# Kernel tuning notes

Measured on AMD Instinct MI355X. Metric: run time of the kernel, lower is better.

Reference implementation:

```python
import jax, jax.numpy as jnp
import numpy as np


def setup_inputs() -> dict:
    key = jax.random.key(0)
    k1, k2 = jax.random.split(key)
    B, D, H, W = 16, 64, 64, 64
    K = 1024  # codebook_size
    x = jax.random.normal(k1, (B, D, H, W), dtype=jnp.float32)
    codebook = jax.random.normal(k2, (K, D), dtype=jnp.float32)
    return {"x": x, "codebook": codebook}


def reference(x, codebook):
    """VQ quantization: nearest-codebook lookup.

    x: (B, D, H, W) latent features; codebook: (K, D).
    Returns (quantized (B, D, H, W), indices (B, H, W)).
    """
    B, D, H, W = x.shape
    # (B, D, H, W) -> (B*H*W, D)
    flat = jnp.transpose(x, (0, 2, 3, 1)).reshape(-1, D)
    d2 = (
        jnp.sum(flat * flat, axis=-1, keepdims=True)
        - 2.0 * (flat @ codebook.T)
        + jnp.sum(codebook * codebook, axis=-1)
    )
    idx = jnp.argmin(d2, axis=-1)  # (N,)
    quantized = codebook[idx]  # (N, D) gather
    quantized = quantized.reshape(B, H, W, D).transpose(0, 3, 1, 2)
    return quantized, idx.reshape(B, H, W)
```

## Files before the change

kernel.cpp:

```cpp
#include <hip/hip_runtime.h>
#include <hip/hip_bf16.h>

#define D_ 64
#define HW_ 4096
#define K_ 1024
#define NPTS_ 65536
#define QOUT_ 4194304
#define DELTA 0.006f
#define INF_ 3.4e38f
#define KSPL 4
#define KPB  256

typedef short bf16x8 __attribute__((ext_vector_type(8)));
typedef float f32x4 __attribute__((ext_vector_type(4)));

__device__ __forceinline__ void gload_lds16(const float* g, float* l) {
    __builtin_amdgcn_global_load_lds((const __attribute__((address_space(1))) void*)g,
                                     (__attribute__((address_space(3))) void*)l, 16, 0, 0);
}
__device__ __forceinline__ void gload_lds4(const float* g, float* l) {
    __builtin_amdgcn_global_load_lds((const __attribute__((address_space(1))) void*)g,
                                     (__attribute__((address_space(3))) void*)l, 4, 0, 0);
}

__global__ __launch_bounds__(256) void vq_pack(const float* __restrict__ cb,
                                               float* __restrict__ cnorm,
                                               short* __restrict__ P) {
    const int t = blockIdx.x * 256 + threadIdx.x;
    const int gch = t >> 6, l = t & 63;
    const int j  = gch * 16 + (l & 15);
    const int dg = l >> 4;
#pragma unroll
    for (int s = 0; s < 2; ++s) {
        const float* src = cb + j * D_ + s * 32 + dg * 8;
        short hb[8], lb[8];
#pragma unroll
        for (int i = 0; i < 8; ++i) {
            const float v = -2.f * src[i];
            __hip_bfloat16 h = __float2bfloat16(v);
            hb[i] = *(const short*)&h;
            const float r = v - __bfloat162float(h);
            __hip_bfloat16 lo = __float2bfloat16(r);
            lb[i] = *(const short*)&lo;
        }
        short* dh = P + ((size_t)((gch * 2 + s) * 2 + 0) * 64 + l) * 8;
        short* dl = P + ((size_t)((gch * 2 + s) * 2 + 1) * 64 + l) * 8;
#pragma unroll
        for (int i = 0; i < 8; ++i) { dh[i] = hb[i]; dl[i] = lb[i]; }
    }
    if (t < K_) {
        const float4* r = (const float4*)(cb + (size_t)t * D_);
        float s0 = 0.f, s1 = 0.f, s2 = 0.f, s3 = 0.f;
#pragma unroll
        for (int i = 0; i < 16; ++i) {
            float4 v = r[i];
            s0 = fmaf(v.x, v.x, s0); s1 = fmaf(v.y, v.y, s1);
            s2 = fmaf(v.z, v.z, s2); s3 = fmaf(v.w, v.w, s3);
        }
        cnorm[t] = (s0 + s1) + (s2 + s3);
    }
}

__global__ __launch_bounds__(512, 4) void vq_main(const float* __restrict__ x,
                                                  const float* __restrict__ cnorm_g,
                                                  const short* __restrict__ P,
                                                  float* __restrict__ out) {
    __shared__ short cbuf[16 * 2 * 2 * 64 * 8];
    __shared__ float cnt[KPB];

    const int tid  = threadIdx.x;
    const int lane = tid & 63;
    const int wid  = tid >> 6;
    const int orig = blockIdx.x;
    const int xcd  = orig & 7;
    const int j    = orig >> 3;
    const int pg   = xcd * 32 + (j & 31);
    const int sp   = j >> 5;
    const int bb   = pg >> 4;
    const int hw0  = (pg & 15) << 8;

    {
        const float* Pf = (const float*)P + (size_t)sp * 16384;
        float* cf = (float*)cbuf;
#pragma unroll
        for (int r = 0; r < 8; ++r)
            gload_lds16(Pf + r * 2048 + wid * 256 + lane * 4, cf + r * 2048 + wid * 256);
        if (wid < 4) gload_lds4(cnorm_g + sp * KPB + wid * 64 + lane, cnt + wid * 64);
    }

    bf16x8 ah[2][2], al[2][2];
    {
        const float* xb = x + (size_t)bb * (D_ * HW_) + hw0;
#pragma unroll
        for (int t = 0; t < 2; ++t) {
            const int p_l = wid * 32 + t * 16 + (lane & 15);
#pragma unroll
            for (int s = 0; s < 2; ++s) {
                const int d0 = s * 32 + (lane >> 4) * 8;
#pragma unroll
                for (int i = 0; i < 8; ++i) {
                    const float v = xb[(size_t)(d0 + i) * HW_ + p_l];
                    __hip_bfloat16 h = __float2bfloat16(v);
                    ah[t][s][i] = *(const short*)&h;
                    const float r = v - __bfloat162float(h);
                    __hip_bfloat16 lo = __float2bfloat16(r);
                    al[t][s][i] = *(const short*)&lo;
                }
            }
        }
    }
    asm volatile("s_waitcnt vmcnt(0)" ::: "memory");
    __syncthreads();

    float m1[8], m2[8];
    int   i1[8];
#pragma unroll
    for (int q = 0; q < 8; ++q) { m1[q] = INF_; m2[q] = INF_; i1[q] = 0; }

    const bf16x8* fr = (const bf16x8*)cbuf;
#pragma unroll 4
    for (int ch = 0; ch < 16; ++ch) {
        const float cn = cnt[ch * 16 + (lane & 15)];
        bf16x8 bh0 = fr[((ch * 2 + 0) * 2 + 0) * 64 + lane];
        bf16x8 bl0 = fr[((ch * 2 + 0) * 2 + 1) * 64 + lane];
        bf16x8 bh1 = fr[((ch * 2 + 1) * 2 + 0) * 64 + lane];
        bf16x8 bl1 = fr[((ch * 2 + 1) * 2 + 1) * 64 + lane];
        f32x4 acc0 = {0.f, 0.f, 0.f, 0.f};
        f32x4 acc1 = {0.f, 0.f, 0.f, 0.f};
        acc0 = __builtin_amdgcn_mfma_f32_16x16x32_bf16(ah[0][0], bh0, acc0, 0, 0, 0);
        acc1 = __builtin_amdgcn_mfma_f32_16x16x32_bf16(ah[1][0], bh0, acc1, 0, 0, 0);
        acc0 = __builtin_amdgcn_mfma_f32_16x16x32_bf16(al[0][0], bh0, acc0, 0, 0, 0);
        acc1 = __builtin_amdgcn_mfma_f32_16x16x32_bf16(al[1][0], bh0, acc1, 0, 0, 0);
        acc0 = __builtin_amdgcn_mfma_f32_16x16x32_bf16(ah[0][0], bl0, acc0, 0, 0, 0);
        acc1 = __builtin_amdgcn_mfma_f32_16x16x32_bf16(ah[1][0], bl0, acc1, 0, 0, 0);
        acc0 = __builtin_amdgcn_mfma_f32_16x16x32_bf16(ah[0][1], bh1, acc0, 0, 0, 0);
        acc1 = __builtin_amdgcn_mfma_f32_16x16x32_bf16(ah[1][1], bh1, acc1, 0, 0, 0);
        acc0 = __builtin_amdgcn_mfma_f32_16x16x32_bf16(al[0][1], bh1, acc0, 0, 0, 0);
        acc1 = __builtin_amdgcn_mfma_f32_16x16x32_bf16(al[1][1], bh1, acc1, 0, 0, 0);
        acc0 = __builtin_amdgcn_mfma_f32_16x16x32_bf16(ah[0][1], bl1, acc0, 0, 0, 0);
        acc1 = __builtin_amdgcn_mfma_f32_16x16x32_bf16(ah[1][1], bl1, acc1, 0, 0, 0);

        const int kc = sp * KPB + ch * 16 + (lane & 15);
#pragma unroll
        for (int t = 0; t < 2; ++t)
#pragma unroll
            for (int r = 0; r < 4; ++r) {
                const int q = t * 4 + r;
                const float d2 = cn + ((t == 0) ? acc0[r] : acc1[r]);
                const bool lt = d2 < m1[q];
                m2[q] = fminf(m2[q], fmaxf(m1[q], d2));
                m1[q] = fminf(m1[q], d2);
                i1[q] = lt ? kc : i1[q];
            }
    }

#pragma unroll
    for (int q = 0; q < 8; ++q) {
        float a1 = m1[q], a2 = m2[q];
        int   ai = i1[q];
#pragma unroll
        for (int m = 1; m < 16; m <<= 1) {
            const float o1 = __shfl_xor(a1, m);
            const int   oi = __shfl_xor(ai, m);
            const float o2 = __shfl_xor(a2, m);
            const float nm2 = fminf(fminf(a2, o2), fmaxf(a1, o1));
            if (o1 < a1 || (o1 == a1 && oi < ai)) { a1 = o1; ai = oi; }
            a2 = nm2;
        }
        if ((lane & 15) == 0) {
            const int t = q >> 2, r = q & 3;
            const int pt = wid * 32 + t * 16 + 4 * (lane >> 4) + r;
            float* cb_col = out + (size_t)bb * (D_ * HW_) + hw0 + pt;
            cb_col[(size_t)(3 * sp + 0) * HW_] = a1;
            cb_col[(size_t)(3 * sp + 1) * HW_] = a2;
            cb_col[(size_t)(3 * sp + 2) * HW_] = (float)ai;
        }
    }
}

__global__ __launch_bounds__(256) void vq_resolve(const float* __restrict__ x,
                                                  const float* __restrict__ cb,
                                                  const float* __restrict__ cnorm_g,
                                                  float* __restrict__ out) {
    __shared__ float tile[64 * 65];
    __shared__ float pp1[4][64];
    __shared__ float pp2[4][64];
    __shared__ int   ppi[4][64];
    __shared__ int   res_idx[64];
    __shared__ int   flist[64];
    __shared__ int   fcnt;

    const int tid  = threadIdx.x;
    const int lane = tid & 63;
    const int wid  = tid >> 6;
    const int orig = blockIdx.x;
    const int qg   = (orig & 7) * 128 + (orig >> 3);
    const int pg   = qg >> 2;
    const int col0 = ((pg & 15) << 8) + ((qg & 3) << 6);
    const int bb   = pg >> 4;
    const int t64  = tid & 63;
    const int s    = tid >> 6;

    if (tid == 0) fcnt = 0;

    const float* rdb = out + (size_t)bb * (D_ * HW_) + col0 + t64;
    const float s1 = rdb[(size_t)(3 * s + 0) * HW_];
    const float s2 = rdb[(size_t)(3 * s + 1) * HW_];
    const int   si = (int)rdb[(size_t)(3 * s + 2) * HW_];
    pp1[s][t64] = s1; pp2[s][t64] = s2; ppi[s][t64] = si;
    __syncthreads();

    if (tid < 64) {
        float b1 = pp1[0][tid], b2 = pp2[0][tid];
        int   bi = ppi[0][tid];
#pragma unroll
        for (int g = 1; g < 4; ++g) {
            const float c1 = pp1[g][tid], c2 = pp2[g][tid];
            const int   ci = ppi[g][tid];
            if (c1 < b1 || (c1 == b1 && ci < bi)) { b2 = fminf(b1, c2); b1 = c1; bi = ci; }
            else                                  { b2 = fminf(b2, fminf(c1, c2)); }
        }
        res_idx[tid] = bi;
        if (b2 - b1 <= DELTA) { const int p = atomicAdd(&fcnt, 1); flist[p] = tid; }
    }
    __syncthreads();

    const int nf = fcnt;
    for (int i = wid; i < nf; i += 4) {
        const int pt = flist[i];
        const float* xr = x + (size_t)bb * (D_ * HW_) + col0 + pt;
        float xv[D_];
#pragma unroll
        for (int d = 0; d < D_; ++d) xv[d] = xr[(size_t)d * HW_];
        float b1 = INF_; int bi = 0;
        for (int c = 0; c < 16; ++c) {
            const int row = lane * 16 + c;
            const float4* cr = (const float4*)(cb + (size_t)row * D_);
            float a0 = 0.f, a1 = 0.f, a2 = 0.f, a3 = 0.f;
#pragma unroll
            for (int g = 0; g < 16; ++g) {
                const float4 cf = cr[g];
                a0 = fmaf(xv[4 * g + 0], cf.x, a0);
                a1 = fmaf(xv[4 * g + 1], cf.y, a1);
                a2 = fmaf(xv[4 * g + 2], cf.z, a2);
                a3 = fmaf(xv[4 * g + 3], cf.w, a3);
            }
            const float dot = (a0 + a1) + (a2 + a3);
            const float d2 = fmaf(-2.f, dot, cnorm_g[row]);
            if (d2 < b1) { b1 = d2; bi = row; }
        }
#pragma unroll
        for (int m = 1; m < 64; m <<= 1) {
            const float o1 = __shfl_xor(b1, m);
            const int   oi = __shfl_xor(bi, m);
            if (o1 < b1 || (o1 == b1 && oi < bi)) { b1 = o1; bi = oi; }
        }
        if (lane == 0) res_idx[pt] = bi;
    }
    __syncthreads();

    if (tid < 64) out[(size_t)QOUT_ + (qg << 6) + tid] = (float)res_idx[tid];

#pragma unroll
    for (int pass = 0; pass < 4; ++pass) {
        const int pt = pass * 16 + (tid >> 4);
        const int dq = tid & 15;
        const float4 v = *(const float4*)(cb + (size_t)res_idx[pt] * D_ + dq * 4);
        float* dst = &tile[pt * 65 + dq * 4];
        dst[0] = v.x; dst[1] = v.y; dst[2] = v.z; dst[3] = v.w;
    }
    __syncthreads();

    float* op = out + (size_t)bb * (D_ * HW_) + col0 + t64;
#pragma unroll
    for (int dd = 0; dd < 16; ++dd) {
        const int d = (tid >> 6) * 16 + dd;
        op[(size_t)d * HW_] = tile[t64 * 65 + d];
    }
}

extern "C" void kernel_launch(void* const* d_in, const int* in_sizes, int n_in,
                              void* d_out, int out_size, void* d_ws, size_t ws_size,
                              hipStream_t stream) {
    const float* x  = (const float*)d_in[0];
    const float* cb = (const float*)d_in[1];
    float* out   = (float*)d_out;
    float* cnorm = (float*)d_ws;
    short* P     = (short*)((char*)d_ws + 4096);

    vq_pack<<<16, 256, 0, stream>>>(cb, cnorm, P);
    vq_main<<<(NPTS_ / 256) * KSPL, 512, 0, stream>>>(x, cnorm, P, out);
    vq_resolve<<<NPTS_ / 64, 256, 0, stream>>>(x, cb, cnorm, out);
}
```

Baseline: 76.73 us.

## Stream full codebook per block with double-buffered LDS instead of K-split partials

The main kernel no longer splits the codebook four ways across blocks. Each 256-thread block now handles 64 points against all 1024 codes, streaming packed codebook chunks through a double-buffered LDS ring with async global-to-LDS loads. It writes a final index, encoded negative when the top-2 margin is ambiguous, so the resolve kernel skips merging four partial results and the scratch traffic through the output buffer. In exchange there is less parallelism per point and a barrier every chunk, and each block rereads the whole codebook from L2.

```diff
diff --git a/kernel.cpp b/kernel.cpp
--- a/kernel.cpp
+++ b/kernel.cpp
@@ -8,8 +8,6 @@
 #define QOUT_ 4194304
 #define DELTA 0.006f
 #define INF_ 3.4e38f
-#define KSPL 4
-#define KPB  256
 
 typedef short bf16x8 __attribute__((ext_vector_type(8)));
 typedef float f32x4 __attribute__((ext_vector_type(4)));
@@ -61,101 +59,99 @@
     }
 }
 
-__global__ __launch_bounds__(512, 4) void vq_main(const float* __restrict__ x,
+__global__ __launch_bounds__(256, 4) void vq_main(const float* __restrict__ x,
                                                   const float* __restrict__ cnorm_g,
                                                   const short* __restrict__ P,
                                                   float* __restrict__ out) {
-    __shared__ short cbuf[16 * 2 * 2 * 64 * 8];
-    __shared__ float cnt[KPB];
+    __shared__ short cbuf[2][4096];
+    __shared__ float cnt[K_];
 
     const int tid  = threadIdx.x;
     const int lane = tid & 63;
     const int wid  = tid >> 6;
-    const int orig = blockIdx.x;
-    const int xcd  = orig & 7;
-    const int j    = orig >> 3;
-    const int pg   = xcd * 32 + (j & 31);
-    const int sp   = j >> 5;
-    const int bb   = pg >> 4;
-    const int hw0  = (pg & 15) << 8;
-
-    {
-        const float* Pf = (const float*)P + (size_t)sp * 16384;
-        float* cf = (float*)cbuf;
-#pragma unroll
-        for (int r = 0; r < 8; ++r)
-            gload_lds16(Pf + r * 2048 + wid * 256 + lane * 4, cf + r * 2048 + wid * 256);
-        if (wid < 4) gload_lds4(cnorm_g + sp * KPB + wid * 64 + lane, cnt + wid * 64);
-    }
-
-    bf16x8 ah[2][2], al[2][2];
+    const int pg   = blockIdx.x;
+    const int bb   = pg >> 6;
+    const int hw0  = (pg & 63) << 6;
+
+    const float* Pf = (const float*)P;
+
+#pragma unroll
+    for (int i = 0; i < 4; ++i)
+        gload_lds4(cnorm_g + i * 256 + wid * 64 + lane, cnt + i * 256 + wid * 64);
+#pragma unroll
+    for (int r = 0; r < 2; ++r)
+        gload_lds16(Pf + r * 1024 + wid * 256 + lane * 4,
+                    (float*)cbuf[0] + r * 1024 + wid * 256);
+
+    bf16x8 ah[2], al[2];
     {
         const float* xb = x + (size_t)bb * (D_ * HW_) + hw0;
-#pragma unroll
-        for (int t = 0; t < 2; ++t) {
-            const int p_l = wid * 32 + t * 16 + (lane & 15);
-#pragma unroll
-            for (int s = 0; s < 2; ++s) {
-                const int d0 = s * 32 + (lane >> 4) * 8;
-#pragma unroll
-                for (int i = 0; i < 8; ++i) {
-                    const float v = xb[(size_t)(d0 + i) * HW_ + p_l];
-                    __hip_bfloat16 h = __float2bfloat16(v);
-                    ah[t][s][i] = *(const short*)&h;
-                    const float r = v - __bfloat162float(h);
-                    __hip_bfloat16 lo = __float2bfloat16(r);
-                    al[t][s][i] = *(const short*)&lo;
-                }
+        const int p_l = wid * 16 + (lane & 15);
+#pragma unroll
+        for (int s = 0; s < 2; ++s) {
+            const int d0 = s * 32 + (lane >> 4) * 8;
+#pragma unroll
+            for (int i = 0; i < 8; ++i) {
+                const float v = xb[(size_t)(d0 + i) * HW_ + p_l];
+                __hip_bfloat16 h = __float2bfloat16(v);
+                ah[s][i] = *(const short*)&h;
+                const float r = v - __bfloat162float(h);
+                __hip_bfloat16 lo = __float2bfloat16(r);
+                al[s][i] = *(const short*)&lo;
             }
         }
     }
     asm volatile("s_waitcnt vmcnt(0)" ::: "memory");
     __syncthreads();
 
-    float m1[8], m2[8];
-    int   i1[8];
-#pragma unroll
-    for (int q = 0; q < 8; ++q) { m1[q] = INF_; m2[q] = INF_; i1[q] = 0; }
-
-    const bf16x8* fr = (const bf16x8*)cbuf;
-#pragma unroll 4
-    for (int ch = 0; ch < 16; ++ch) {
-        const float cn = cnt[ch * 16 + (lane & 15)];
-        bf16x8 bh0 = fr[((ch * 2 + 0) * 2 + 0) * 64 + lane];
-        bf16x8 bl0 = fr[((ch * 2 + 0) * 2 + 1) * 64 + lane];
-        bf16x8 bh1 = fr[((ch * 2 + 1) * 2 + 0) * 64 + lane];
-        bf16x8 bl1 = fr[((ch * 2 + 1) * 2 + 1) * 64 + lane];
-        f32x4 acc0 = {0.f, 0.f, 0.f, 0.f};
-        f32x4 acc1 = {0.f, 0.f, 0.f, 0.f};
-        acc0 = __builtin_amdgcn_mfma_f32_16x16x32_bf16(ah[0][0], bh0, acc0, 0, 0, 0);
-        acc1 = __builtin_amdgcn_mfma_f32_16x16x32_bf16(ah[1][0], bh0, acc1, 0, 0, 0);
-        acc0 = __builtin_amdgcn_mfma_f32_16x16x32_bf16(al[0][0], bh0, acc0, 0, 0, 0);
-        acc1 = __builtin_amdgcn_mfma_f32_16x16x32_bf16(al[1][0], bh0, acc1, 0, 0, 0);
-        acc0 = __builtin_amdgcn_mfma_f32_16x16x32_bf16(ah[0][0], bl0, acc0, 0, 0, 0);
-        acc1 = __builtin_amdgcn_mfma_f32_16x16x32_bf16(ah[1][0], bl0, acc1, 0, 0, 0);
-        acc0 = __builtin_amdgcn_mfma_f32_16x16x32_bf16(ah[0][1], bh1, acc0, 0, 0, 0);
-        acc1 = __builtin_amdgcn_mfma_f32_16x16x32_bf16(ah[1][1], bh1, acc1, 0, 0, 0);
-        acc0 = __builtin_amdgcn_mfma_f32_16x16x32_bf16(al[0][1], bh1, acc0, 0, 0, 0);
-        acc1 = __builtin_amdgcn_mfma_f32_16x16x32_bf16(al[1][1], bh1, acc1, 0, 0, 0);
-        acc0 = __builtin_amdgcn_mfma_f32_16x16x32_bf16(ah[0][1], bl1, acc0, 0, 0, 0);
-        acc1 = __builtin_amdgcn_mfma_f32_16x16x32_bf16(ah[1][1], bl1, acc1, 0, 0, 0);
-
-        const int kc = sp * KPB + ch * 16 + (lane & 15);
-#pragma unroll
-        for (int t = 0; t < 2; ++t)
+    float m1[4], m2[4];
+    int   i1[4];
+#pragma unroll
+    for (int q = 0; q < 4; ++q) { m1[q] = INF_; m2[q] = INF_; i1[q] = 0; }
+
+    int cur = 0;
+#pragma unroll 1
+    for (int c = 0; c < 32; ++c) {
+        if (c + 1 < 32) {
+            const float* src = Pf + (size_t)(c + 1) * 2048;
+            float* dst = (float*)cbuf[cur ^ 1];
+#pragma unroll
+            for (int r = 0; r < 2; ++r)
+                gload_lds16(src + r * 1024 + wid * 256 + lane * 4,
+                            dst + r * 1024 + wid * 256);
+        }
+        const bf16x8* fr = (const bf16x8*)cbuf[cur];
+#pragma unroll
+        for (int u = 0; u < 2; ++u) {
+            const int kc = c * 32 + u * 16 + (lane & 15);
+            const float cn = cnt[kc];
+            bf16x8 bh0 = fr[(u * 4 + 0) * 64 + lane];
+            bf16x8 bl0 = fr[(u * 4 + 1) * 64 + lane];
+            bf16x8 bh1 = fr[(u * 4 + 2) * 64 + lane];
+            bf16x8 bl1 = fr[(u * 4 + 3) * 64 + lane];
+            f32x4 aa = {0.f, 0.f, 0.f, 0.f};
+            f32x4 ab = {0.f, 0.f, 0.f, 0.f};
+            aa = __builtin_amdgcn_mfma_f32_16x16x32_bf16(ah[0], bh0, aa, 0, 0, 0);
+            ab = __builtin_amdgcn_mfma_f32_16x16x32_bf16(ah[1], bh1, ab, 0, 0, 0);
+            aa = __builtin_amdgcn_mfma_f32_16x16x32_bf16(al[0], bh0, aa, 0, 0, 0);
+            ab = __builtin_amdgcn_mfma_f32_16x16x32_bf16(al[1], bh1, ab, 0, 0, 0);
+            aa = __builtin_amdgcn_mfma_f32_16x16x32_bf16(ah[0], bl0, aa, 0, 0, 0);
+            ab = __builtin_amdgcn_mfma_f32_16x16x32_bf16(ah[1], bl1, ab, 0, 0, 0);
 #pragma unroll
             for (int r = 0; r < 4; ++r) {
-                const int q = t * 4 + r;
-                const float d2 = cn + ((t == 0) ? acc0[r] : acc1[r]);
-                const bool lt = d2 < m1[q];
-                m2[q] = fminf(m2[q], fmaxf(m1[q], d2));
-                m1[q] = fminf(m1[q], d2);
-                i1[q] = lt ? kc : i1[q];
+                const float d2 = cn + (aa[r] + ab[r]);
+                const bool lt = d2 < m1[r];
+                m2[r] = fminf(m2[r], fmaxf(m1[r], d2));
+                m1[r] = fminf(m1[r], d2);
+                i1[r] = lt ? kc : i1[r];
             }
-    }
-
-#pragma unroll
-    for (int q = 0; q < 8; ++q) {
+        }
+        __syncthreads();
+        cur ^= 1;
+    }
+
+#pragma unroll
+    for (int q = 0; q < 4; ++q) {
         float a1 = m1[q], a2 = m2[q];
         int   ai = i1[q];
 #pragma unroll
@@ -168,12 +164,9 @@
             a2 = nm2;
         }
         if ((lane & 15) == 0) {
-            const int t = q >> 2, r = q & 3;
-            const int pt = wid * 32 + t * 16 + 4 * (lane >> 4) + r;
-            float* cb_col = out + (size_t)bb * (D_ * HW_) + hw0 + pt;
-            cb_col[(size_t)(3 * sp + 0) * HW_] = a1;
-            cb_col[(size_t)(3 * sp + 1) * HW_] = a2;
-            cb_col[(size_t)(3 * sp + 2) * HW_] = (float)ai;
+            const int pt = wid * 16 + 4 * (lane >> 4) + q;
+            const bool amb = (a2 - a1 <= DELTA);
+            out[(size_t)QOUT_ + pg * 64 + pt] = amb ? -(float)(ai + 1) : (float)ai;
         }
     }
 }
@@ -183,45 +176,26 @@
                                                   const float* __restrict__ cnorm_g,
                                                   float* __restrict__ out) {
     __shared__ float tile[64 * 65];
-    __shared__ float pp1[4][64];
-    __shared__ float pp2[4][64];
-    __shared__ int   ppi[4][64];
-    __shared__ int   res_idx[64];
-    __shared__ int   flist[64];
-    __shared__ int   fcnt;
+    __shared__ int res_idx[64];
+    __shared__ int flist[64];
+    __shared__ int fcnt;
 
     const int tid  = threadIdx.x;
     const int lane = tid & 63;
     const int wid  = tid >> 6;
-    const int orig = blockIdx.x;
-    const int qg   = (orig & 7) * 128 + (orig >> 3);
-    const int pg   = qg >> 2;
-    const int col0 = ((pg & 15) << 8) + ((qg & 3) << 6);
-    const int bb   = pg >> 4;
+    const int qg   = blockIdx.x;
+    const int bb   = qg >> 6;
+    const int col0 = (qg & 63) << 6;
     const int t64  = tid & 63;
-    const int s    = tid >> 6;
 
     if (tid == 0) fcnt = 0;
-
-    const float* rdb = out + (size_t)bb * (D_ * HW_) + col0 + t64;
-    const float s1 = rdb[(size_t)(3 * s + 0) * HW_];
-    const float s2 = rdb[(size_t)(3 * s + 1) * HW_];
-    const int   si = (int)rdb[(size_t)(3 * s + 2) * HW_];
-    pp1[s][t64] = s1; pp2[s][t64] = s2; ppi[s][t64] = si;
     __syncthreads();
 
     if (tid < 64) {
-        float b1 = pp1[0][tid], b2 = pp2[0][tid];
-        int   bi = ppi[0][tid];
-#pragma unroll
-        for (int g = 1; g < 4; ++g) {
-            const float c1 = pp1[g][tid], c2 = pp2[g][tid];
-            const int   ci = ppi[g][tid];
-            if (c1 < b1 || (c1 == b1 && ci < bi)) { b2 = fminf(b1, c2); b1 = c1; bi = ci; }
-            else                                  { b2 = fminf(b2, fminf(c1, c2)); }
-        }
-        res_idx[tid] = bi;
-        if (b2 - b1 <= DELTA) { const int p = atomicAdd(&fcnt, 1); flist[p] = tid; }
+        const float v = out[(size_t)QOUT_ + qg * 64 + tid];
+        const bool fl = v < 0.f;
+        res_idx[tid] = fl ? (int)(-v) - 1 : (int)v;
+        if (fl) { const int p = atomicAdd(&fcnt, 1); flist[p] = tid; }
     }
     __syncthreads();
 
@@ -259,7 +233,7 @@
     }
     __syncthreads();
 
-    if (tid < 64) out[(size_t)QOUT_ + (qg << 6) + tid] = (float)res_idx[tid];
+    if (tid < 64) out[(size_t)QOUT_ + qg * 64 + tid] = (float)res_idx[tid];
 
 #pragma unroll
     for (int pass = 0; pass < 4; ++pass) {
@@ -289,6 +263,6 @@
     short* P     = (short*)((char*)d_ws + 4096);
 
     vq_pack<<<16, 256, 0, stream>>>(cb, cnorm, P);
-    vq_main<<<(NPTS_ / 256) * KSPL, 512, 0, stream>>>(x, cnorm, P, out);
+    vq_main<<<NPTS_ / 64, 256, 0, stream>>>(x, cnorm, P, out);
     vq_resolve<<<NPTS_ / 64, 256, 0, stream>>>(x, cb, cnorm, out);
 }
```

Result: no change. 76.23 us (-0.7%).
